# Performance work log

Measured on AMD Instinct MI355X. Metric: run time of the kernel, lower is better.

The kernel has to match this reference:

```python
import jax, jax.numpy as jnp
import numpy as np

B, S, D, H, N = 4, 2048, 512, 8, 64
HD = D // H  # head dim


def setup_inputs() -> dict:
    key = jax.random.key(0)
    ks = jax.random.split(key, 4)
    s = 0.02  # xavier-ish init scale
    return {
        "x": jax.random.normal(ks[0], (B, S, D), jnp.float32),
        "in_proj_w": jax.random.normal(ks[1], (3 * D, D), jnp.float32) * s,
        "in_proj_b": jnp.zeros((3 * D,), jnp.float32),
        "out_proj_w": jax.random.normal(ks[2], (D, D), jnp.float32) * s,
        "out_proj_b": jnp.zeros((D,), jnp.float32),
        "content_w": jax.random.normal(ks[3], (N, D), jnp.float32) * s,
        "content_b": jnp.zeros((N,), jnp.float32),
        "k_input": 16,
    }


def _fwd_core(x, in_proj_w, in_proj_b, out_proj_w, out_proj_b, content_w, content_b):
    # torch nn.MultiheadAttention (batch_first, eval/no dropout), self-attention
    qkv = jnp.einsum("bsd,ed->bse", x, in_proj_w) + in_proj_b  # [B,S,3D]
    q, k, v = jnp.split(qkv, 3, axis=-1)
    to_heads = lambda t: t.reshape(B, S, H, HD).transpose(0, 2, 1, 3)  # [B,H,S,hd]
    q, k, v = to_heads(q), to_heads(k), to_heads(v)
    scores = jnp.einsum("bhqd,bhkd->bhqk", q, k) / jnp.sqrt(jnp.float32(HD))
    attn = jax.nn.softmax(scores, axis=-1)  # [B,H,S,S] (need_weights=True path)
    ctx = jnp.einsum("bhqk,bhkd->bhqd", attn, v)
    ctx = ctx.transpose(0, 2, 1, 3).reshape(B, S, D)
    attended = jnp.einsum("bsd,ed->bse", ctx, out_proj_w) + out_proj_b  # [B,S,D]

    # content_to_neuron
    aff = jnp.einsum("bsd,nd->bsn", attended, content_w) + content_b  # [B,S,N]

    # position importance: mean over heads, sum over keys, normalize
    pos_imp = attn.mean(axis=1).sum(axis=2)  # [B,S]
    pos_imp = pos_imp / (pos_imp.sum(axis=1, keepdims=True) + 1e-8)

    weighted = (aff * pos_imp[..., None]).sum(axis=1)  # [B,N]
    final = 0.5 * weighted + 0.3 * aff.max(axis=1) + 0.2 * aff.mean(axis=1)
    probs = jax.nn.softmax(final, axis=-1)
    return final, probs, attended


def reference(x, in_proj_w, in_proj_b, out_proj_w, out_proj_b, content_w, content_b, k_input):
    final, probs, attended = _fwd_core(
        x, in_proj_w, in_proj_b, out_proj_w, out_proj_b, content_w, content_b
    )
    _, input_idx = jax.lax.top_k(final, k_input)  # [B,k]
    one_hot = jnp.zeros_like(probs).at[jnp.arange(B)[:, None], input_idx].set(1.0)
    # straight-through: value == one_hot, gradient flows through probs
    routing_weights = jax.lax.stop_gradient(one_hot - probs) + probs
    return input_idx, routing_weights, attended
```

## Files before the change

kernel.cpp:

```cpp
#include <hip/hip_runtime.h>
#include <hip/hip_bf16.h>

typedef unsigned short u16;
typedef __bf16 bf16x8 __attribute__((ext_vector_type(8)));
typedef u16 u16x8 __attribute__((ext_vector_type(8)));
typedef u16 u16x4 __attribute__((ext_vector_type(4)));
typedef float f32x4 __attribute__((ext_vector_type(4)));

__device__ __forceinline__ u16 f2bf(float f) {
  union { float f; unsigned u; } v; v.f = f;
  return (u16)((v.u + 0x7FFFu + ((v.u >> 16) & 1u)) >> 16);
}
__device__ __forceinline__ float bf2f(u16 h) {
  union { unsigned u; float f; } v; v.u = ((unsigned)h) << 16;
  return v.f;
}
struct BfPair { u16 hi, lo; };
__device__ __forceinline__ BfPair split2(float f) {
  BfPair r;
  r.hi = f2bf(f);
  r.lo = f2bf(f - bf2f(r.hi));
  return r;
}
__device__ __forceinline__ bf16x8 as_bf16x8(u16x8 u) {
  union { u16x8 u; bf16x8 b; } v; v.u = u; return v.b;
}

#define MFMA16(a, b, c) __builtin_amdgcn_mfma_f32_16x16x32_bf16((a), (b), (c), 0, 0, 0)

#define GLD16(gp, lp)                                                          \
  __builtin_amdgcn_global_load_lds(                                            \
      (const __attribute__((address_space(1))) void*)(gp),                     \
      (__attribute__((address_space(3))) void*)(lp), 16, 0, 0)

__global__ __launch_bounds__(256) void split_kernel(
    const float* __restrict__ src, u16* __restrict__ hi, u16* __restrict__ lo, int n4)
{
  int i = blockIdx.x * 256 + threadIdx.x;
  if (i >= n4) return;
  f32x4 v = ((const f32x4*)src)[i];
  u16x4 h, l;
  #pragma unroll
  for (int j = 0; j < 4; j++) { BfPair p = split2(v[j]); h[j] = p.hi; l[j] = p.lo; }
  ((u16x4*)hi)[i] = h;
  ((u16x4*)lo)[i] = l;
}

template<int OUT_PLANES>
__global__ __launch_bounds__(256, 3) void gemm_nt(
    const u16* __restrict__ Ah, const u16* __restrict__ Al,
    const u16* __restrict__ Bh, const u16* __restrict__ Bl,
    const float* __restrict__ bias,
    void* __restrict__ C0, void* __restrict__ C1,
    int M, int N, int K)
{
  __shared__ u16 Ash[128 * 32], Asl[128 * 32];
  __shared__ u16 Bsh[128 * 32], Bsl[128 * 32];
  const int t = threadIdx.x;
  const int lane = t & 63, w = t >> 6;
  const int l15 = lane & 15, g = lane >> 4;
  const int m0 = blockIdx.x * 128, n0 = blockIdx.y * 128;

  const int lrow = lane >> 2;
  const int lchunk = lane & 3;

  f32x4 acc[4][4] = {};

  for (int k0 = 0; k0 < K; k0 += 32) {
    __syncthreads();
    #pragma unroll
    for (int q = 0; q < 2; q++) {
      const int row = w * 32 + q * 16 + lrow;
      const int sw = lchunk ^ (row & 3) ^ ((row >> 2) & 3);
      const size_t ga = (size_t)(m0 + row) * K + k0 + sw * 8;
      const size_t gb = (size_t)(n0 + row) * K + k0 + sw * 8;
      const int ldsbase = (w * 32 + q * 16) * 32;
      GLD16(Ah + ga, &Ash[ldsbase]);
      GLD16(Al + ga, &Asl[ldsbase]);
      GLD16(Bh + gb, &Bsh[ldsbase]);
      GLD16(Bl + gb, &Bsl[ldsbase]);
    }
    __syncthreads();

    bf16x8 bh[4], bl[4];
    #pragma unroll
    for (int n = 0; n < 4; n++) {
      const int row = (w & 1) * 64 + n * 16 + l15;
      const int slot = g ^ (row & 3) ^ ((row >> 2) & 3);
      const int idx = row * 32 + slot * 8;
      bh[n] = *(const bf16x8*)&Bsh[idx];
      bl[n] = *(const bf16x8*)&Bsl[idx];
    }
    #pragma unroll
    for (int m = 0; m < 4; m++) {
      const int row = (w >> 1) * 64 + m * 16 + l15;
      const int slot = g ^ (row & 3) ^ ((row >> 2) & 3);
      const int idx = row * 32 + slot * 8;
      bf16x8 ah = *(const bf16x8*)&Ash[idx];
      bf16x8 al = *(const bf16x8*)&Asl[idx];
      #pragma unroll
      for (int n = 0; n < 4; n++) {
        acc[m][n] = MFMA16(ah, bh[n], acc[m][n]);
        acc[m][n] = MFMA16(ah, bl[n], acc[m][n]);
        acc[m][n] = MFMA16(al, bh[n], acc[m][n]);
      }
    }
  }

  const int r0 = m0 + (w >> 1) * 64;
  const int c0 = n0 + (w & 1) * 64;
  float bs[4];
  #pragma unroll
  for (int n = 0; n < 4; n++) bs[n] = bias[c0 + n * 16 + l15];
  #pragma unroll
  for (int m = 0; m < 4; m++)
    #pragma unroll
    for (int n = 0; n < 4; n++) {
      const int col = c0 + n * 16 + l15;
      #pragma unroll
      for (int r = 0; r < 4; r++) {
        float v = acc[m][n][r] + bs[n];
        size_t idx = (size_t)(r0 + m * 16 + g * 4 + r) * N + col;
        if (OUT_PLANES) {
          BfPair pp = split2(v);
          ((u16*)C0)[idx] = pp.hi;
          ((u16*)C1)[idx] = pp.lo;
        } else {
          ((float*)C0)[idx] = v;
        }
      }
    }
}

__global__ __launch_bounds__(256, 2) void attn_kernel(
    const u16* __restrict__ qkv_h, const u16* __restrict__ qkv_l,
    u16* __restrict__ ctx_h, u16* __restrict__ ctx_l)
{
  const int bh = blockIdx.x;
  const int b = bh >> 3, h = bh & 7;
  const int q0 = blockIdx.y * 128;
  const int t = threadIdx.x, lane = t & 63, w = t >> 6;
  const int l15 = lane & 15, g = lane >> 4;

  __shared__ u16 Ksh[64 * 72], Ksl[64 * 72];
  __shared__ u16 Vsh[64 * 72], Vsl[64 * 72];
  __shared__ u16 Psh[4][32 * 72], Psl[4][32 * 72];

  const size_t rowbase = (size_t)b * 2048;

  bf16x8 qbh[2][2], qbl[2][2];
  #pragma unroll
  for (int i = 0; i < 2; i++) {
    size_t qoff = (rowbase + q0 + i * 64 + w * 16 + l15) * 1536 + h * 64 + g * 8;
    #pragma unroll
    for (int kc = 0; kc < 2; kc++) {
      u16x8 uh = *(const u16x8*)(qkv_h + qoff + kc * 32);
      u16x8 ul = *(const u16x8*)(qkv_l + qoff + kc * 32);
      #pragma unroll
      for (int j = 0; j < 8; j++) {
        uh[j] = f2bf(bf2f(uh[j]) * 0.125f);
        ul[j] = f2bf(bf2f(ul[j]) * 0.125f);
      }
      qbh[i][kc] = as_bf16x8(uh);
      qbl[i][kc] = as_bf16x8(ul);
    }
  }

  f32x4 oacc[2][4] = {};
  float l_q[2] = {0.f, 0.f};

  u16x8 skh[2], skl[2], svh[2], svl[2];
  #pragma unroll
  for (int rep = 0; rep < 2; rep++) {
    int c = t + rep * 256;
    int row = c >> 3, col = (c & 7) * 8;
    size_t off = (rowbase + row) * 1536 + h * 64 + col;
    skh[rep] = *(const u16x8*)(qkv_h + off + 512);
    skl[rep] = *(const u16x8*)(qkv_l + off + 512);
    svh[rep] = *(const u16x8*)(qkv_h + off + 1024);
    svl[rep] = *(const u16x8*)(qkv_l + off + 1024);
  }

  for (int kt = 0; kt < 32; kt++) {
    __syncthreads();
    #pragma unroll
    for (int rep = 0; rep < 2; rep++) {
      int c = t + rep * 256;
      int row = c >> 3, col = (c & 7) * 8;
      *(u16x8*)&Ksh[row * 72 + col] = skh[rep];
      *(u16x8*)&Ksl[row * 72 + col] = skl[rep];
      int rk = (row + col) & 63;
      #pragma unroll
      for (int j = 0; j < 8; j++) {
        Vsh[(col + j) * 72 + rk] = svh[rep][j];
        Vsl[(col + j) * 72 + rk] = svl[rep][j];
      }
    }
    if (kt + 1 < 32) {
      #pragma unroll
      for (int rep = 0; rep < 2; rep++) {
        int c = t + rep * 256;
        int row = c >> 3, col = (c & 7) * 8;
        size_t off = (rowbase + (kt + 1) * 64 + row) * 1536 + h * 64 + col;
        skh[rep] = *(const u16x8*)(qkv_h + off + 512);
        skl[rep] = *(const u16x8*)(qkv_l + off + 512);
        svh[rep] = *(const u16x8*)(qkv_h + off + 1024);
        svl[rep] = *(const u16x8*)(qkv_l + off + 1024);
      }
    }
    __syncthreads();

    f32x4 sa0[4] = {}, sa1[4] = {};
    #pragma unroll
    for (int kc = 0; kc < 2; kc++) {
      #pragma unroll
      for (int cb = 0; cb < 4; cb++) {
        int ki = (cb * 16 + l15) * 72 + g * 8 + kc * 32;
        bf16x8 kh = *(const bf16x8*)&Ksh[ki];
        bf16x8 kl = *(const bf16x8*)&Ksl[ki];
        sa0[cb] = MFMA16(kh, qbh[0][kc], sa0[cb]);
        sa1[cb] = MFMA16(kh, qbh[1][kc], sa1[cb]);
        sa0[cb] = MFMA16(kh, qbl[0][kc], sa0[cb]);
        sa1[cb] = MFMA16(kh, qbl[1][kc], sa1[cb]);
        sa0[cb] = MFMA16(kl, qbh[0][kc], sa0[cb]);
        sa1[cb] = MFMA16(kl, qbh[1][kc], sa1[cb]);
      }
    }

    #pragma unroll
    for (int i = 0; i < 2; i++) {
      f32x4* sa = (i == 0) ? sa0 : sa1;
      float rs = 0.f;
      #pragma unroll
      for (int cb = 0; cb < 4; cb++)
        #pragma unroll
        for (int r = 0; r < 4; r++) {
          float p = __expf(sa[cb][r]);
          sa[cb][r] = p;
          rs += p;
        }
      rs += __shfl_xor(rs, 16, 64);
      rs += __shfl_xor(rs, 32, 64);
      l_q[i] += rs;

      #pragma unroll
      for (int cb = 0; cb < 4; cb++) {
        u16x4 ph, pl;
        #pragma unroll
        for (int r = 0; r < 4; r++) {
          BfPair pp = split2(sa[cb][r]);
          ph[r] = pp.hi; pl[r] = pp.lo;
        }
        int pi = (i * 16 + l15) * 72 + cb * 16 + g * 4;
        *(u16x4*)&Psh[w][pi] = ph;
        *(u16x4*)&Psl[w][pi] = pl;
      }
    }

    asm volatile("s_waitcnt lgkmcnt(0)" ::: "memory");
    __builtin_amdgcn_sched_barrier(0);

    bf16x8 pah[2][2], pal[2][2];
    #pragma unroll
    for (int i = 0; i < 2; i++)
      #pragma unroll
      for (int kc = 0; kc < 2; kc++) {
        int pb = (i * 16 + l15) * 72 + kc * 32 + g * 8;
        pah[i][kc] = *(const bf16x8*)&Psh[w][pb];
        pal[i][kc] = *(const bf16x8*)&Psl[w][pb];
      }

    #pragma unroll
    for (int kc = 0; kc < 2; kc++) {
      #pragma unroll
      for (int cb = 0; cb < 4; cb++) {
        int d = cb * 16 + l15;
        int rk0 = (g * 8 + kc * 32 + (d & 56)) & 63;
        bf16x8 vbh = *(const bf16x8*)&Vsh[d * 72 + rk0];
        bf16x8 vbl = *(const bf16x8*)&Vsl[d * 72 + rk0];
        oacc[0][cb] = MFMA16(pah[0][kc], vbh, oacc[0][cb]);
        oacc[1][cb] = MFMA16(pah[1][kc], vbh, oacc[1][cb]);
        oacc[0][cb] = MFMA16(pah[0][kc], vbl, oacc[0][cb]);
        oacc[1][cb] = MFMA16(pah[1][kc], vbl, oacc[1][cb]);
        oacc[0][cb] = MFMA16(pal[0][kc], vbh, oacc[0][cb]);
        oacc[1][cb] = MFMA16(pal[1][kc], vbh, oacc[1][cb]);
      }
    }
  }

  #pragma unroll
  for (int i = 0; i < 2; i++)
    #pragma unroll
    for (int r = 0; r < 4; r++) {
      float lq = __shfl(l_q[i], g * 4 + r, 64);
      float inv = 1.0f / lq;
      int row = q0 + i * 64 + w * 16 + g * 4 + r;
      size_t base = (rowbase + row) * 512 + h * 64;
      #pragma unroll
      for (int cb = 0; cb < 4; cb++) {
        BfPair pp = split2(oacc[i][cb][r] * inv);
        ctx_h[base + cb * 16 + l15] = pp.hi;
        ctx_l[base + cb * 16 + l15] = pp.lo;
      }
    }
}

__global__ __launch_bounds__(256) void aff_reduce(
    const float* __restrict__ att, const float* __restrict__ cw,
    const float* __restrict__ cbias, float* __restrict__ psum, float* __restrict__ pmax)
{
  const int b = blockIdx.x, sb = blockIdx.y;
  const int t = threadIdx.x;
  const int n = t & 63, rg = t >> 6;
  __shared__ float cws[64 * 65];
  __shared__ float ats[32 * 65];
  __shared__ float reds[256], redm[256];

  float acc[8] = {};
  for (int kc = 0; kc < 8; kc++) {
    __syncthreads();
    #pragma unroll
    for (int i = 0; i < 4; i++) {
      int c = t + i * 256;
      int row = c >> 4, col = (c & 15) * 4;
      f32x4 v = *(const f32x4*)(cw + (size_t)row * 512 + kc * 64 + col);
      cws[row * 65 + col + 0] = v[0]; cws[row * 65 + col + 1] = v[1];
      cws[row * 65 + col + 2] = v[2]; cws[row * 65 + col + 3] = v[3];
    }
    #pragma unroll
    for (int i = 0; i < 2; i++) {
      int c = t + i * 256;
      int row = c >> 4, col = (c & 15) * 4;
      f32x4 v = *(const f32x4*)(att + ((size_t)b * 2048 + sb * 32 + row) * 512 + kc * 64 + col);
      ats[row * 65 + col + 0] = v[0]; ats[row * 65 + col + 1] = v[1];
      ats[row * 65 + col + 2] = v[2]; ats[row * 65 + col + 3] = v[3];
    }
    __syncthreads();
    for (int k = 0; k < 64; k++) {
      float c = cws[n * 65 + k];
      #pragma unroll
      for (int r = 0; r < 8; r++)
        acc[r] += ats[(rg * 8 + r) * 65 + k] * c;
    }
  }
  const float bn = cbias[n];
  float s = 0.f, m = -1e30f;
  #pragma unroll
  for (int r = 0; r < 8; r++) {
    float v = acc[r] + bn;
    s += v; m = fmaxf(m, v);
  }
  reds[t] = s; redm[t] = m;
  __syncthreads();
  if (t < 64) {
    float ss = reds[t] + reds[64 + t] + reds[128 + t] + reds[192 + t];
    float mm = fmaxf(fmaxf(redm[t], redm[64 + t]), fmaxf(redm[128 + t], redm[192 + t]));
    psum[((size_t)b * 64 + sb) * 64 + t] = ss;
    pmax[((size_t)b * 64 + sb) * 64 + t] = mm;
  }
}

__global__ void final_topk(const float* __restrict__ psum, const float* __restrict__ pmax,
                           float* __restrict__ out)
{
  __shared__ float fin[4][64];
  const int t = threadIdx.x;
  const int b = t >> 6, n = t & 63;
  float s = 0.f, m = -1e30f;
  for (int j = 0; j < 64; j++) {
    s += psum[((size_t)b * 64 + j) * 64 + n];
    m = fmaxf(m, pmax[((size_t)b * 64 + j) * 64 + n]);
  }
  const float mean = s * (1.0f / 2048.0f);
  fin[b][n] = 0.5f * mean + 0.3f * m + 0.2f * mean;
  __syncthreads();
  if (t < 4) {
    unsigned long long chosen = 0ull;
    for (int j = 0; j < 16; j++) {
      float best = -3e38f; int bi = 0;
      for (int nn = 0; nn < 64; nn++) {
        float v = fin[t][nn];
        if (!((chosen >> nn) & 1ull) && v > best) { best = v; bi = nn; }
      }
      chosen |= 1ull << bi;
      out[t * 16 + j] = (float)bi;
    }
    for (int nn = 0; nn < 64; nn++)
      out[64 + t * 64 + nn] = ((chosen >> nn) & 1ull) ? 1.0f : 0.0f;
  }
}

extern "C" void kernel_launch(void* const* d_in, const int* in_sizes, int n_in,
                              void* d_out, int out_size, void* d_ws, size_t ws_size,
                              hipStream_t stream) {
  const float* x    = (const float*)d_in[0];
  const float* win  = (const float*)d_in[1];
  const float* bin  = (const float*)d_in[2];
  const float* wout = (const float*)d_in[3];
  const float* bout = (const float*)d_in[4];
  const float* cw   = (const float*)d_in[5];
  const float* cbv  = (const float*)d_in[6];
  (void)in_sizes; (void)n_in; (void)ws_size; (void)out_size;

  float* out = (float*)d_out;
  char* ws = (char*)d_ws;
  u16*   qkv_h = (u16*)ws;
  u16*   qkv_l = (u16*)(ws + 25165824);
  u16*   ctx_h = (u16*)(ws + 50331648);
  u16*   ctx_l = (u16*)(ws + 58720256);
  float* psum  = (float*)(ws + 67108864);
  float* pmax  = (float*)(ws + 67174400);
  u16*   winh  = (u16*)(ws + 67239936);
  u16*   winl  = (u16*)(ws + 68812800);
  u16*   wouth = (u16*)(ws + 70385664);
  u16*   woutl = (u16*)(ws + 70909952);
  u16*   xh = ctx_h, *xl = ctx_l;
  float* attended = out + 320;

  split_kernel<<<4096, 256, 0, stream>>>(x, xh, xl, 1048576);
  split_kernel<<<768, 256, 0, stream>>>(win, winh, winl, 196608);
  split_kernel<<<256, 256, 0, stream>>>(wout, wouth, woutl, 65536);

  gemm_nt<1><<<dim3(64, 12), 256, 0, stream>>>(
      xh, xl, winh, winl, bin, qkv_h, qkv_l, 8192, 1536, 512);
  attn_kernel<<<dim3(32, 16), 256, 0, stream>>>(qkv_h, qkv_l, ctx_h, ctx_l);
  gemm_nt<0><<<dim3(64, 4), 256, 0, stream>>>(
      ctx_h, ctx_l, wouth, woutl, bout, attended, nullptr, 8192, 512, 512);
  aff_reduce<<<dim3(4, 64), 256, 0, stream>>>(attended, cw, cbv, psum, pmax);
  final_topk<<<1, 256, 0, stream>>>(psum, pmax, out);
}
```

Measured before the change: 283.6 us.

## Widen attention blocks to 8 waves sharing K/V tiles, packed bf16 P conversion

The attention kernel now runs 512 threads covering 256 query rows per block, so each K/V tile staged in shared memory serves twice as many queries and global K/V traffic is halved. Each thread loads one K/V chunk instead of two. The softmax uses exp2 with log2e folded into the Q scale, and the hi/lo bf16 split of P uses packed v_cvt_pk_bf16_f32. The P hi and lo planes are staged through a single shared buffer one after the other, which halves P's shared-memory footprint but adds an extra wait and round trip. The grid drops to 256 blocks, which may lower occupancy and load balance across CUs.

```diff
diff --git a/kernel.cpp b/kernel.cpp
--- a/kernel.cpp
+++ b/kernel.cpp
@@ -2,6 +2,7 @@
 #include <hip/hip_bf16.h>
 
 typedef unsigned short u16;
+typedef unsigned int u32;
 typedef __bf16 bf16x8 __attribute__((ext_vector_type(8)));
 typedef u16 u16x8 __attribute__((ext_vector_type(8)));
 typedef u16 u16x4 __attribute__((ext_vector_type(4)));
@@ -14,6 +15,9 @@
 __device__ __forceinline__ float bf2f(u16 h) {
   union { unsigned u; float f; } v; v.u = ((unsigned)h) << 16;
   return v.f;
+}
+__device__ __forceinline__ float asf(u32 u) {
+  union { unsigned u; float f; } v; v.u = u; return v.f;
 }
 struct BfPair { u16 hi, lo; };
 __device__ __forceinline__ BfPair split2(float f) {
@@ -24,6 +28,11 @@
 }
 __device__ __forceinline__ bf16x8 as_bf16x8(u16x8 u) {
   union { u16x8 u; bf16x8 b; } v; v.u = u; return v.b;
+}
+__device__ __forceinline__ u32 cvt_pk(float a, float b) {
+  u32 r;
+  asm volatile("v_cvt_pk_bf16_f32 %0, %1, %2" : "=v"(r) : "v"(a), "v"(b));
+  return r;
 }
 
 #define MFMA16(a, b, c) __builtin_amdgcn_mfma_f32_16x16x32_bf16((a), (b), (c), 0, 0, 0)
@@ -60,7 +69,6 @@
   const int lane = t & 63, w = t >> 6;
   const int l15 = lane & 15, g = lane >> 4;
   const int m0 = blockIdx.x * 128, n0 = blockIdx.y * 128;
-
   const int lrow = lane >> 2;
   const int lchunk = lane & 3;
 
@@ -132,34 +140,37 @@
     }
 }
 
-__global__ __launch_bounds__(256, 2) void attn_kernel(
+__global__ __launch_bounds__(512, 2) void attn_kernel(
     const u16* __restrict__ qkv_h, const u16* __restrict__ qkv_l,
     u16* __restrict__ ctx_h, u16* __restrict__ ctx_l)
 {
   const int bh = blockIdx.x;
   const int b = bh >> 3, h = bh & 7;
-  const int q0 = blockIdx.y * 128;
+  const int q0 = blockIdx.y * 256;
   const int t = threadIdx.x, lane = t & 63, w = t >> 6;
   const int l15 = lane & 15, g = lane >> 4;
+  const int wh = w >> 2, wl = w & 3;
 
   __shared__ u16 Ksh[64 * 72], Ksl[64 * 72];
   __shared__ u16 Vsh[64 * 72], Vsl[64 * 72];
-  __shared__ u16 Psh[4][32 * 72], Psl[4][32 * 72];
+  __shared__ u16 Ps[8][32 * 72];
 
   const size_t rowbase = (size_t)b * 2048;
+  const float QSC = 0.125f * 1.44269504088896f;
 
   bf16x8 qbh[2][2], qbl[2][2];
   #pragma unroll
   for (int i = 0; i < 2; i++) {
-    size_t qoff = (rowbase + q0 + i * 64 + w * 16 + l15) * 1536 + h * 64 + g * 8;
+    size_t qoff = (rowbase + q0 + wh * 128 + i * 64 + wl * 16 + l15) * 1536 + h * 64 + g * 8;
     #pragma unroll
     for (int kc = 0; kc < 2; kc++) {
       u16x8 uh = *(const u16x8*)(qkv_h + qoff + kc * 32);
       u16x8 ul = *(const u16x8*)(qkv_l + qoff + kc * 32);
       #pragma unroll
       for (int j = 0; j < 8; j++) {
-        uh[j] = f2bf(bf2f(uh[j]) * 0.125f);
-        ul[j] = f2bf(bf2f(ul[j]) * 0.125f);
+        float v = (bf2f(uh[j]) + bf2f(ul[j])) * QSC;
+        BfPair p = split2(v);
+        uh[j] = p.hi; ul[j] = p.lo;
       }
       qbh[i][kc] = as_bf16x8(uh);
       qbl[i][kc] = as_bf16x8(ul);
@@ -169,44 +180,34 @@
   f32x4 oacc[2][4] = {};
   float l_q[2] = {0.f, 0.f};
 
-  u16x8 skh[2], skl[2], svh[2], svl[2];
-  #pragma unroll
-  for (int rep = 0; rep < 2; rep++) {
-    int c = t + rep * 256;
-    int row = c >> 3, col = (c & 7) * 8;
-    size_t off = (rowbase + row) * 1536 + h * 64 + col;
-    skh[rep] = *(const u16x8*)(qkv_h + off + 512);
-    skl[rep] = *(const u16x8*)(qkv_l + off + 512);
-    svh[rep] = *(const u16x8*)(qkv_h + off + 1024);
-    svl[rep] = *(const u16x8*)(qkv_l + off + 1024);
+  const int srow = t >> 3, scol = (t & 7) * 8;
+  u16x8 skh, skl, svh, svl;
+  {
+    size_t off = (rowbase + srow) * 1536 + h * 64 + scol;
+    skh = *(const u16x8*)(qkv_h + off + 512);
+    skl = *(const u16x8*)(qkv_l + off + 512);
+    svh = *(const u16x8*)(qkv_h + off + 1024);
+    svl = *(const u16x8*)(qkv_l + off + 1024);
   }
 
   for (int kt = 0; kt < 32; kt++) {
     __syncthreads();
-    #pragma unroll
-    for (int rep = 0; rep < 2; rep++) {
-      int c = t + rep * 256;
-      int row = c >> 3, col = (c & 7) * 8;
-      *(u16x8*)&Ksh[row * 72 + col] = skh[rep];
-      *(u16x8*)&Ksl[row * 72 + col] = skl[rep];
-      int rk = (row + col) & 63;
+    {
+      *(u16x8*)&Ksh[srow * 72 + scol] = skh;
+      *(u16x8*)&Ksl[srow * 72 + scol] = skl;
+      int rk = (srow + scol) & 63;
       #pragma unroll
       for (int j = 0; j < 8; j++) {
-        Vsh[(col + j) * 72 + rk] = svh[rep][j];
-        Vsl[(col + j) * 72 + rk] = svl[rep][j];
+        Vsh[(scol + j) * 72 + rk] = svh[j];
+        Vsl[(scol + j) * 72 + rk] = svl[j];
       }
     }
     if (kt + 1 < 32) {
-      #pragma unroll
-      for (int rep = 0; rep < 2; rep++) {
-        int c = t + rep * 256;
-        int row = c >> 3, col = (c & 7) * 8;
-        size_t off = (rowbase + (kt + 1) * 64 + row) * 1536 + h * 64 + col;
-        skh[rep] = *(const u16x8*)(qkv_h + off + 512);
-        skl[rep] = *(const u16x8*)(qkv_l + off + 512);
-        svh[rep] = *(const u16x8*)(qkv_h + off + 1024);
-        svl[rep] = *(const u16x8*)(qkv_l + off + 1024);
-      }
+      size_t off = (rowbase + (kt + 1) * 64 + srow) * 1536 + h * 64 + scol;
+      skh = *(const u16x8*)(qkv_h + off + 512);
+      skl = *(const u16x8*)(qkv_l + off + 512);
+      svh = *(const u16x8*)(qkv_h + off + 1024);
+      svl = *(const u16x8*)(qkv_l + off + 1024);
     }
     __syncthreads();
 
@@ -227,48 +228,64 @@
       }
     }
 
+    u32 hw[2][4][2], lw[2][4][2];
     #pragma unroll
     for (int i = 0; i < 2; i++) {
       f32x4* sa = (i == 0) ? sa0 : sa1;
       float rs = 0.f;
       #pragma unroll
-      for (int cb = 0; cb < 4; cb++)
+      for (int cb = 0; cb < 4; cb++) {
         #pragma unroll
         for (int r = 0; r < 4; r++) {
-          float p = __expf(sa[cb][r]);
+          float p = exp2f(sa[cb][r]);
           sa[cb][r] = p;
           rs += p;
         }
+        u32 h0 = cvt_pk(sa[cb][0], sa[cb][1]);
+        u32 h1 = cvt_pk(sa[cb][2], sa[cb][3]);
+        hw[i][cb][0] = h0; hw[i][cb][1] = h1;
+        float l0 = sa[cb][0] - asf(h0 << 16);
+        float l1 = sa[cb][1] - asf(h0 & 0xFFFF0000u);
+        float l2 = sa[cb][2] - asf(h1 << 16);
+        float l3 = sa[cb][3] - asf(h1 & 0xFFFF0000u);
+        lw[i][cb][0] = cvt_pk(l0, l1);
+        lw[i][cb][1] = cvt_pk(l2, l3);
+      }
       rs += __shfl_xor(rs, 16, 64);
       rs += __shfl_xor(rs, 32, 64);
       l_q[i] += rs;
-
-      #pragma unroll
-      for (int cb = 0; cb < 4; cb++) {
-        u16x4 ph, pl;
-        #pragma unroll
-        for (int r = 0; r < 4; r++) {
-          BfPair pp = split2(sa[cb][r]);
-          ph[r] = pp.hi; pl[r] = pp.lo;
-        }
-        int pi = (i * 16 + l15) * 72 + cb * 16 + g * 4;
-        *(u16x4*)&Psh[w][pi] = ph;
-        *(u16x4*)&Psl[w][pi] = pl;
-      }
-    }
-
+    }
+
+    #pragma unroll
+    for (int i = 0; i < 2; i++)
+      #pragma unroll
+      for (int cb = 0; cb < 4; cb++) {
+        u32* dst = (u32*)&Ps[w][(i * 16 + l15) * 72 + cb * 16 + g * 4];
+        dst[0] = hw[i][cb][0]; dst[1] = hw[i][cb][1];
+      }
     asm volatile("s_waitcnt lgkmcnt(0)" ::: "memory");
     __builtin_amdgcn_sched_barrier(0);
-
     bf16x8 pah[2][2], pal[2][2];
     #pragma unroll
     for (int i = 0; i < 2; i++)
       #pragma unroll
-      for (int kc = 0; kc < 2; kc++) {
-        int pb = (i * 16 + l15) * 72 + kc * 32 + g * 8;
-        pah[i][kc] = *(const bf16x8*)&Psh[w][pb];
-        pal[i][kc] = *(const bf16x8*)&Psl[w][pb];
-      }
+      for (int kc = 0; kc < 2; kc++)
+        pah[i][kc] = *(const bf16x8*)&Ps[w][(i * 16 + l15) * 72 + kc * 32 + g * 8];
+    __builtin_amdgcn_sched_barrier(0);
+    #pragma unroll
+    for (int i = 0; i < 2; i++)
+      #pragma unroll
+      for (int cb = 0; cb < 4; cb++) {
+        u32* dst = (u32*)&Ps[w][(i * 16 + l15) * 72 + cb * 16 + g * 4];
+        dst[0] = lw[i][cb][0]; dst[1] = lw[i][cb][1];
+      }
+    asm volatile("s_waitcnt lgkmcnt(0)" ::: "memory");
+    __builtin_amdgcn_sched_barrier(0);
+    #pragma unroll
+    for (int i = 0; i < 2; i++)
+      #pragma unroll
+      for (int kc = 0; kc < 2; kc++)
+        pal[i][kc] = *(const bf16x8*)&Ps[w][(i * 16 + l15) * 72 + kc * 32 + g * 8];
 
     #pragma unroll
     for (int kc = 0; kc < 2; kc++) {
@@ -294,7 +311,7 @@
     for (int r = 0; r < 4; r++) {
       float lq = __shfl(l_q[i], g * 4 + r, 64);
       float inv = 1.0f / lq;
-      int row = q0 + i * 64 + w * 16 + g * 4 + r;
+      int row = q0 + wh * 128 + i * 64 + wl * 16 + g * 4 + r;
       size_t base = (rowbase + row) * 512 + h * 64;
       #pragma unroll
       for (int cb = 0; cb < 4; cb++) {
@@ -423,7 +440,7 @@
 
   gemm_nt<1><<<dim3(64, 12), 256, 0, stream>>>(
       xh, xl, winh, winl, bin, qkv_h, qkv_l, 8192, 1536, 512);
-  attn_kernel<<<dim3(32, 16), 256, 0, stream>>>(qkv_h, qkv_l, ctx_h, ctx_l);
+  attn_kernel<<<dim3(32, 8), 512, 0, stream>>>(qkv_h, qkv_l, ctx_h, ctx_l);
   gemm_nt<0><<<dim3(64, 4), 256, 0, stream>>>(
       ctx_h, ctx_l, wouth, woutl, bout, attended, nullptr, 8192, 512, 512);
   aff_reduce<<<dim3(4, 64), 256, 0, stream>>>(attended, cw, cbv, psum, pmax);
```

After: 268.4 us, median of 3. 1.06x faster.
